# Kernel tuning notes

Measured on AMD Instinct MI355X. Metric: run time of the kernel, lower is better.

## Reference

```python
import jax, jax.numpy as jnp
import numpy as np
import math

B, L, S, E, D = 32, 2048, 2048, 64, 64

def setup_inputs() -> dict:
    key = jax.random.key(0)
    kq, kk, kv = jax.random.split(key, 3)
    return {
        "queries": jax.random.normal(kq, (B, L, E), dtype=jnp.float32),
        "keys":    jax.random.normal(kk, (B, S, E), dtype=jnp.float32),
        "values":  jax.random.normal(kv, (B, S, D), dtype=jnp.float32),
    }

def reference(queries, keys, values):
    # scale = 1/sqrt(E) since self.scale is None
    scale = 1.0 / math.sqrt(queries.shape[-1])
    # unfused QK^T -> softmax -> V (dropout is identity at inference)
    scores = jnp.einsum('ble,bse->bls', queries, keys)  # [B,L,S]
    # mask_flag branch not taken because L == S (matches torch code path)
    A = jax.nn.softmax(scale * scores, axis=-1)
    V = jnp.einsum('bls,bsd->bld', A, values)  # [B,L,D]
    return V
```

## Files before the change

### kernel.cpp

```cpp
#include <hip/hip_runtime.h>
#include <hip/hip_bf16.h>


#define B_ 32
#define L_ 2048
#define S_ 2048
#define E_ 64
#define D_ 64
#define BQ 128
#define NIMG 32
#define IMG_BYTES 16384
#define NCHUNK 16

typedef __attribute__((ext_vector_type(8))) short bf16x8;
typedef __attribute__((ext_vector_type(16))) float f32x16;
typedef __attribute__((ext_vector_type(4))) unsigned u32x4;

__device__ __forceinline__ unsigned short f2b(float f) {
  unsigned u = __builtin_bit_cast(unsigned, f);
  u += 0x7fff + ((u >> 16) & 1);
  return (unsigned short)(u >> 16);
}

__device__ __forceinline__ unsigned pk2(float a, float b) {
#if defined(__has_builtin) && __has_builtin(__builtin_amdgcn_cvt_pk_bf16_f32)
  typedef __bf16 b2 __attribute__((ext_vector_type(2)));
  b2 t = __builtin_amdgcn_cvt_pk_bf16_f32(a, b);
  return __builtin_bit_cast(unsigned, t);
#else
  return (unsigned)f2b(a) | ((unsigned)f2b(b) << 16);
#endif
}

__device__ __forceinline__ float fexp2(float x) {
#if defined(__has_builtin) && __has_builtin(__builtin_amdgcn_exp2f)
  return __builtin_amdgcn_exp2f(x);
#else
  return exp2f(x);
#endif
}

__device__ __forceinline__ void cp16(const void* g, void* lbase) {
#if defined(__has_builtin) && __has_builtin(__builtin_amdgcn_global_load_lds)
  typedef const __attribute__((address_space(1))) void gvoid;
  typedef __attribute__((address_space(3))) void lvoid;
  __builtin_amdgcn_global_load_lds((gvoid*)g, (lvoid*)lbase, 16, 0, 0);
#endif
}

__global__ __launch_bounds__(256) void prepass(
    const float* __restrict__ K, const float* __restrict__ V,
    char* __restrict__ ws) {
  const int tid  = threadIdx.x;
  const int lane = tid & 63;
  const int quad = lane >> 4;
  const int qb0  = quad & 1;
  const int qb1  = (quad >> 1) & 1;

  const int b  = blockIdx.x >> 5;
  const int c  = blockIdx.x & 31;
  const int s0 = c * 64;

  const float* Kb = K + (long)b * S_ * E_;
  const float* Vb = V + (long)b * S_ * D_;
  short* img = (short*)(ws + (size_t)blockIdx.x * IMG_BYTES);

#pragma unroll
  for (int it = 0; it < 4; ++it) {
    const int i  = tid + it * 256;
    const int s  = i >> 4;
    const int c4 = (i & 15) << 2;

    float4 kv = *(const float4*)(Kb + (long)(s0 + s) * E_ + c4);
    {
      int g = ((c4 >> 3) + s) & 7;
      *(uint2*)&img[s * 64 + g * 8 + (c4 & 7)] = make_uint2(pk2(kv.x, kv.y), pk2(kv.z, kv.w));
    }

    float4 vv = *(const float4*)(Vb + (long)(s0 + s) * D_ + c4);
    float a0 = vv.x, a1 = vv.y, a2 = vv.z, a3 = vv.w;
    float s0f = qb1 ? a0 : a2;
    float s1f = qb1 ? a1 : a3;
    float r0  = __shfl_xor(s0f, 32);
    float r1  = __shfl_xor(s1f, 32);
    float b0 = qb1 ? r0 : a0;
    float b1 = qb1 ? r1 : a1;
    float b2 = qb1 ? a2 : r0;
    float b3 = qb1 ? a3 : r1;
    float t0 = qb0 ? b0 : b1;
    float t1 = qb0 ? b2 : b3;
    float u0 = __shfl_xor(t0, 16);
    float u1 = __shfl_xor(t1, 16);
    float w0 = qb0 ? u0 : b0;
    float w1 = qb0 ? b1 : u0;
    float w2 = qb0 ? u1 : b2;
    float w3 = qb0 ? b3 : u1;
    const int base = s - quad;
    const int d    = c4 + quad;
    int g = ((base >> 3) + d) & 7;
    *(uint2*)&img[4096 + d * 64 + g * 8 + (base & 7)] = make_uint2(pk2(w0, w1), pk2(w2, w3));
  }
}

__global__ __launch_bounds__(512, 4) void attn_fwd(
    const float* __restrict__ Q, const char* __restrict__ ws,
    float* __restrict__ O) {
  __shared__ __align__(16) char smem[65536 + 1024];
  float* Obuf = (float*)smem;
  float* ML   = (float*)(smem + 65536);

  const int tid  = threadIdx.x;
  const int lane = tid & 63;
  const int wv   = tid >> 6;
  const int l31  = lane & 31;
  const int h    = lane >> 5;
  const int qg   = wv >> 1;
  const int kh   = wv & 1;

  const int b  = blockIdx.x >> 4;
  const int q0 = (blockIdx.x & 15) * BQ;

  const float SCALE2 = 0.125f * 1.44269504088896340736f;
  const char* img0 = ws + (size_t)b * ((size_t)NIMG * IMG_BYTES);

#pragma unroll
  for (int j = 0; j < 4; ++j)
    cp16(img0 + wv * 4096 + j * 1024 + lane * 16, smem + wv * 4096 + j * 1024);

  bf16x8 qf[4];
  {
    const float* qrow = Q + ((long)b * L_ + q0 + qg * 32 + l31) * E_;
#pragma unroll
    for (int ke = 0; ke < 4; ++ke) {
      const float* sp = qrow + ke * 16 + h * 8;
      float4 x = *(const float4*)(sp);
      float4 y = *(const float4*)(sp + 4);
      u32x4 uu = { pk2(x.x * SCALE2, x.y * SCALE2), pk2(x.z * SCALE2, x.w * SCALE2),
                   pk2(y.x * SCALE2, y.y * SCALE2), pk2(y.z * SCALE2, y.w * SCALE2) };
      qf[ke] = __builtin_bit_cast(bf16x8, uu);
    }
  }

  int pl = l31;
  {
    const int blk = (pl >> 2) & 3;
    if (blk == 1) pl += 4;
    else if (blk == 2) pl -= 4;
  }

  int offK[2][4];
#pragma unroll
  for (int nt = 0; nt < 2; ++nt) {
    const int row = nt * 32 + pl;
#pragma unroll
    for (int ke = 0; ke < 4; ++ke)
      offK[nt][ke] = kh * 16384 + row * 128 + (((ke * 2 + h) + row) & 7) * 16;
  }
  int offV[2][4];
#pragma unroll
  for (int mt = 0; mt < 2; ++mt) {
    const int d = mt * 32 + l31;
#pragma unroll
    for (int ks = 0; ks < 4; ++ks)
      offV[mt][ks] = kh * 16384 + 8192 + d * 128 + (((ks * 2 + h) + d) & 7) * 16;
  }

  f32x16 o[2];
#pragma unroll
  for (int mt = 0; mt < 2; ++mt)
#pragma unroll
    for (int r = 0; r < 16; ++r) o[mt][r] = 0.f;
  float lrun = 0.f;

  __syncthreads();

#define CHUNK_BODY(TT, BUFB, OTHB)                                             \
  {                                                                            \
    if ((TT) + 1 < NCHUNK) {                                                   \
      const char* img = img0 + (size_t)((TT) + 1) * 32768;                     \
      _Pragma("unroll")                                                        \
      for (int j = 0; j < 4; ++j)                                              \
        cp16(img + wv * 4096 + j * 1024 + lane * 16,                           \
             smem + (OTHB) + wv * 4096 + j * 1024);                            \
    }                                                                          \
    _Pragma("unroll")                                                          \
    for (int nt = 0; nt < 2; ++nt) {                                           \
      bf16x8 kf[4];                                                            \
      _Pragma("unroll")                                                        \
      for (int ke = 0; ke < 4; ++ke)                                           \
        kf[ke] = *(const bf16x8*)(smem + (BUFB) + offK[nt][ke]);               \
      f32x16 acc;                                                              \
      _Pragma("unroll")                                                        \
      for (int r = 0; r < 16; ++r) acc[r] = 0.f;                               \
      _Pragma("unroll")                                                        \
      for (int ke = 0; ke < 4; ++ke)                                           \
        acc = __builtin_amdgcn_mfma_f32_32x32x16_bf16(kf[ke], qf[ke], acc,     \
                                                      0, 0, 0);                \
      float pr[16];                                                            \
      _Pragma("unroll")                                                        \
      for (int r = 0; r < 16; ++r) pr[r] = fexp2(acc[r]);                      \
      float rsa = 0.f, rsb = 0.f;                                              \
      _Pragma("unroll")                                                        \
      for (int r = 0; r < 8; ++r) { rsa += pr[2 * r]; rsb += pr[2 * r + 1]; }  \
      lrun += rsa + rsb;                                                       \
      u32x4 f0 = { pk2(pr[0], pr[1]), pk2(pr[2], pr[3]),                       \
                   pk2(pr[4], pr[5]), pk2(pr[6], pr[7]) };                     \
      bf16x8 pf0 = __builtin_bit_cast(bf16x8, f0);                             \
      u32x4 f1 = { pk2(pr[8], pr[9]), pk2(pr[10], pr[11]),                     \
                   pk2(pr[12], pr[13]), pk2(pr[14], pr[15]) };                 \
      bf16x8 pf1 = __builtin_bit_cast(bf16x8, f1);                             \
      _Pragma("unroll")                                                        \
      for (int mt = 0; mt < 2; ++mt) {                                         \
        bf16x8 vf0 = *(const bf16x8*)(smem + (BUFB) + offV[mt][nt * 2 + 0]);   \
        o[mt] = __builtin_amdgcn_mfma_f32_32x32x16_bf16(vf0, pf0, o[mt],       \
                                                        0, 0, 0);              \
        bf16x8 vf1 = *(const bf16x8*)(smem + (BUFB) + offV[mt][nt * 2 + 1]);   \
        o[mt] = __builtin_amdgcn_mfma_f32_32x32x16_bf16(vf1, pf1, o[mt],       \
                                                        0, 0, 0);              \
      }                                                                        \
    }                                                                          \
    __syncthreads();                                                           \
  }

  for (int t = 0; t < NCHUNK; t += 2) {
    CHUNK_BODY(t, 0, 32768)
    CHUNK_BODY(t + 1, 32768, 0)
  }
#undef CHUNK_BODY

  float lt = lrun + __shfl_xor(lrun, 32);

  if (lane < 32)
    ML[(qg * 2 + kh) * 32 + l31] = lt;
  __syncthreads();

  const float inv = 1.f / (lt + ML[(qg * 2 + (kh ^ 1)) * 32 + l31]);
  const int q = qg * 32 + l31;

  if (kh == 1) {
#pragma unroll
    for (int mt = 0; mt < 2; ++mt)
#pragma unroll
      for (int r = 0; r < 16; ++r) {
        const int d = mt * 32 + (r & 3) + 8 * (r >> 2) + 4 * h;
        Obuf[q * 68 + d] = o[mt][r];
      }
  }
  __syncthreads();

  if (kh == 0) {
#pragma unroll
    for (int mt = 0; mt < 2; ++mt)
#pragma unroll
      for (int r = 0; r < 16; ++r) {
        const int d = mt * 32 + (r & 3) + 8 * (r >> 2) + 4 * h;
        Obuf[q * 68 + d] = (o[mt][r] + Obuf[q * 68 + d]) * inv;
      }
  }
  __syncthreads();

  {
    const int qq = tid >> 2;
    const int dh = (tid & 3) * 16;
    float* orow = O + ((long)b * L_ + q0 + qq) * D_ + dh;
    const float* src = &Obuf[qq * 68 + dh];
#pragma unroll
    for (int j = 0; j < 4; ++j)
      *(float4*)(orow + j * 4) = *(const float4*)(src + j * 4);
  }
}

extern "C" void kernel_launch(void* const* d_in, const int* in_sizes, int n_in,
                              void* d_out, int out_size, void* d_ws, size_t ws_size,
                              hipStream_t stream) {
  const float* Q = (const float*)d_in[0];
  const float* K = (const float*)d_in[1];
  const float* V = (const float*)d_in[2];
  float* O = (float*)d_out;

  prepass<<<dim3(B_ * NIMG), dim3(256), 0, stream>>>(K, V, (char*)d_ws);
  attn_fwd<<<dim3(B_ * (L_ / BQ)), dim3(512), 0, stream>>>(Q, (const char*)d_ws, O);
}
```

Baseline: 150.2 us.

## Replace barrier double-buffering with flag-synced 4-stage producer/consumer LDS ring

Each tile now holds 64 keys, split across the two key-halves, instead of two images per stage. A 4-buffer LDS ring is managed by per-buffer ready and consumed counters in shared memory instead of block-wide __syncthreads. A rotating producer wave waits for a buffer to be drained, then issues global_load_lds for the chunk four steps ahead and sets its ready flag. The K/V swizzle changes from additive to XOR so LDS addresses reduce to XORs of a base offset. The aim is to drop per-chunk full-block barriers and let waves drift apart. The spin-waits rely on volatile LDS polling and the order of s_waitcnt, which risks stalls or races.

```diff
diff --git a/kernel.cpp b/kernel.cpp
--- a/kernel.cpp
+++ b/kernel.cpp
@@ -10,7 +10,8 @@
 #define BQ 128
 #define NIMG 32
 #define IMG_BYTES 16384
-#define NCHUNK 16
+#define NCHUNK 32
+#define NBUF 4
 
 typedef __attribute__((ext_vector_type(8))) short bf16x8;
 typedef __attribute__((ext_vector_type(16))) float f32x16;
@@ -48,6 +49,10 @@
 #endif
 }
 
+__device__ __forceinline__ void wait_ge(const volatile int* p, int want) {
+  while (*p < want) __builtin_amdgcn_s_sleep(1);
+}
+
 __global__ __launch_bounds__(256) void prepass(
     const float* __restrict__ K, const float* __restrict__ V,
     char* __restrict__ ws) {
@@ -73,7 +78,7 @@
 
     float4 kv = *(const float4*)(Kb + (long)(s0 + s) * E_ + c4);
     {
-      int g = ((c4 >> 3) + s) & 7;
+      int g = (c4 >> 3) ^ (s & 7);
       *(uint2*)&img[s * 64 + g * 8 + (c4 & 7)] = make_uint2(pk2(kv.x, kv.y), pk2(kv.z, kv.w));
     }
 
@@ -97,7 +102,7 @@
     float w3 = qb0 ? b3 : u1;
     const int base = s - quad;
     const int d    = c4 + quad;
-    int g = ((base >> 3) + d) & 7;
+    int g = (base >> 3) ^ (d & 7);
     *(uint2*)&img[4096 + d * 64 + g * 8 + (base & 7)] = make_uint2(pk2(w0, w1), pk2(w2, w3));
   }
 }
@@ -105,9 +110,10 @@
 __global__ __launch_bounds__(512, 4) void attn_fwd(
     const float* __restrict__ Q, const char* __restrict__ ws,
     float* __restrict__ O) {
-  __shared__ __align__(16) char smem[65536 + 1024];
+  __shared__ __align__(16) char smem[65536 + 1024 + 64];
   float* Obuf = (float*)smem;
   float* ML   = (float*)(smem + 65536);
+  int*   sync = (int*)(smem + 66560);
 
   const int tid  = threadIdx.x;
   const int lane = tid & 63;
@@ -123,9 +129,15 @@
   const float SCALE2 = 0.125f * 1.44269504088896340736f;
   const char* img0 = ws + (size_t)b * ((size_t)NIMG * IMG_BYTES);
 
-#pragma unroll
-  for (int j = 0; j < 4; ++j)
-    cp16(img0 + wv * 4096 + j * 1024 + lane * 16, smem + wv * 4096 + j * 1024);
+  if (tid < 8) sync[tid] = 0;
+  __syncthreads();
+
+  if (wv < 4) {
+    const char* img = img0 + (size_t)wv * IMG_BYTES;
+#pragma unroll
+    for (int j = 0; j < 16; ++j)
+      cp16(img + j * 1024 + lane * 16, smem + wv * 16384 + j * 1024);
+  }
 
   bf16x8 qf[4];
   {
@@ -141,6 +153,11 @@
     }
   }
 
+  if (wv < 4) {
+    asm volatile("s_waitcnt vmcnt(0)" ::: "memory");
+    if (lane == 0) ((volatile int*)sync)[wv] = 1;
+  }
+
   int pl = l31;
   {
     const int blk = (pl >> 2) & 3;
@@ -148,22 +165,8 @@
     else if (blk == 2) pl -= 4;
   }
 
-  int offK[2][4];
-#pragma unroll
-  for (int nt = 0; nt < 2; ++nt) {
-    const int row = nt * 32 + pl;
-#pragma unroll
-    for (int ke = 0; ke < 4; ++ke)
-      offK[nt][ke] = kh * 16384 + row * 128 + (((ke * 2 + h) + row) & 7) * 16;
-  }
-  int offV[2][4];
-#pragma unroll
-  for (int mt = 0; mt < 2; ++mt) {
-    const int d = mt * 32 + l31;
-#pragma unroll
-    for (int ks = 0; ks < 4; ++ks)
-      offV[mt][ks] = kh * 16384 + 8192 + d * 128 + (((ks * 2 + h) + d) & 7) * 16;
-  }
+  const int kb = (kh << 12) + (pl << 7) + ((h ^ (pl & 7)) << 4);
+  const int vb = 8192 + (l31 << 7) + (((kh * 4 + h) ^ (l31 & 7)) << 4);
 
   f32x16 o[2];
 #pragma unroll
@@ -172,61 +175,65 @@
     for (int r = 0; r < 16; ++r) o[mt][r] = 0.f;
   float lrun = 0.f;
 
-  __syncthreads();
-
-#define CHUNK_BODY(TT, BUFB, OTHB)                                             \
-  {                                                                            \
-    if ((TT) + 1 < NCHUNK) {                                                   \
-      const char* img = img0 + (size_t)((TT) + 1) * 32768;                     \
-      _Pragma("unroll")                                                        \
-      for (int j = 0; j < 4; ++j)                                              \
-        cp16(img + wv * 4096 + j * 1024 + lane * 16,                           \
-             smem + (OTHB) + wv * 4096 + j * 1024);                            \
-    }                                                                          \
-    _Pragma("unroll")                                                          \
-    for (int nt = 0; nt < 2; ++nt) {                                           \
-      bf16x8 kf[4];                                                            \
-      _Pragma("unroll")                                                        \
-      for (int ke = 0; ke < 4; ++ke)                                           \
-        kf[ke] = *(const bf16x8*)(smem + (BUFB) + offK[nt][ke]);               \
-      f32x16 acc;                                                              \
-      _Pragma("unroll")                                                        \
-      for (int r = 0; r < 16; ++r) acc[r] = 0.f;                               \
-      _Pragma("unroll")                                                        \
-      for (int ke = 0; ke < 4; ++ke)                                           \
-        acc = __builtin_amdgcn_mfma_f32_32x32x16_bf16(kf[ke], qf[ke], acc,     \
-                                                      0, 0, 0);                \
-      float pr[16];                                                            \
-      _Pragma("unroll")                                                        \
-      for (int r = 0; r < 16; ++r) pr[r] = fexp2(acc[r]);                      \
-      float rsa = 0.f, rsb = 0.f;                                              \
-      _Pragma("unroll")                                                        \
-      for (int r = 0; r < 8; ++r) { rsa += pr[2 * r]; rsb += pr[2 * r + 1]; }  \
-      lrun += rsa + rsb;                                                       \
-      u32x4 f0 = { pk2(pr[0], pr[1]), pk2(pr[2], pr[3]),                       \
-                   pk2(pr[4], pr[5]), pk2(pr[6], pr[7]) };                     \
-      bf16x8 pf0 = __builtin_bit_cast(bf16x8, f0);                             \
-      u32x4 f1 = { pk2(pr[8], pr[9]), pk2(pr[10], pr[11]),                     \
-                   pk2(pr[12], pr[13]), pk2(pr[14], pr[15]) };                 \
-      bf16x8 pf1 = __builtin_bit_cast(bf16x8, f1);                             \
-      _Pragma("unroll")                                                        \
-      for (int mt = 0; mt < 2; ++mt) {                                         \
-        bf16x8 vf0 = *(const bf16x8*)(smem + (BUFB) + offV[mt][nt * 2 + 0]);   \
-        o[mt] = __builtin_amdgcn_mfma_f32_32x32x16_bf16(vf0, pf0, o[mt],       \
-                                                        0, 0, 0);              \
-        bf16x8 vf1 = *(const bf16x8*)(smem + (BUFB) + offV[mt][nt * 2 + 1]);   \
-        o[mt] = __builtin_amdgcn_mfma_f32_32x32x16_bf16(vf1, pf1, o[mt],       \
-                                                        0, 0, 0);              \
-      }                                                                        \
-    }                                                                          \
-    __syncthreads();                                                           \
-  }
-
-  for (int t = 0; t < NCHUNK; t += 2) {
-    CHUNK_BODY(t, 0, 32768)
-    CHUNK_BODY(t + 1, 32768, 0)
-  }
-#undef CHUNK_BODY
+  for (int t = 0; t < NCHUNK; ++t) {
+    const int s = t & 3;
+    wait_ge((volatile int*)&sync[s], (t >> 2) + 1);
+    asm volatile("" ::: "memory");
+
+    const int bufb = s << 14;
+    const int kbuf = kb ^ bufb;
+    const int vbuf = vb ^ bufb;
+
+    bf16x8 kf[4];
+#pragma unroll
+    for (int ke = 0; ke < 4; ++ke)
+      kf[ke] = *(const bf16x8*)(smem + (kbuf ^ (ke << 5)));
+    f32x16 acc;
+#pragma unroll
+    for (int r = 0; r < 16; ++r) acc[r] = 0.f;
+#pragma unroll
+    for (int ke = 0; ke < 4; ++ke)
+      acc = __builtin_amdgcn_mfma_f32_32x32x16_bf16(kf[ke], qf[ke], acc, 0, 0, 0);
+
+    u32x4 f0, f1;
+#pragma unroll
+    for (int g = 0; g < 4; ++g) {
+      float p0 = fexp2(acc[2 * g]);
+      float p1 = fexp2(acc[2 * g + 1]);
+      lrun += p0 + p1;
+      f0[g] = pk2(p0, p1);
+      float p2 = fexp2(acc[8 + 2 * g]);
+      float p3 = fexp2(acc[8 + 2 * g + 1]);
+      lrun += p2 + p3;
+      f1[g] = pk2(p2, p3);
+    }
+    bf16x8 pf0 = __builtin_bit_cast(bf16x8, f0);
+    bf16x8 pf1 = __builtin_bit_cast(bf16x8, f1);
+
+#pragma unroll
+    for (int mt = 0; mt < 2; ++mt) {
+      bf16x8 vf0 = *(const bf16x8*)(smem + (vbuf ^ (mt << 12)));
+      o[mt] = __builtin_amdgcn_mfma_f32_32x32x16_bf16(vf0, pf0, o[mt], 0, 0, 0);
+      bf16x8 vf1 = *(const bf16x8*)(smem + (vbuf ^ (mt << 12) ^ (1 << 5)));
+      o[mt] = __builtin_amdgcn_mfma_f32_32x32x16_bf16(vf1, pf1, o[mt], 0, 0, 0);
+    }
+
+    asm volatile("s_waitcnt lgkmcnt(0)" ::: "memory");
+    if (lane == 0) atomicAdd(&sync[4 + s], 1);
+
+    const int tp = t + 4;
+    if (tp < NCHUNK && (tp & 7) == wv) {
+      const int sp_ = tp & 3;
+      wait_ge((volatile int*)&sync[4 + sp_], (tp >> 2) * 8);
+      asm volatile("" ::: "memory");
+      const char* img = img0 + (size_t)tp * IMG_BYTES;
+#pragma unroll
+      for (int j = 0; j < 16; ++j)
+        cp16(img + j * 1024 + lane * 16, smem + sp_ * 16384 + j * 1024);
+      asm volatile("s_waitcnt vmcnt(0)" ::: "memory");
+      if (lane == 0) ((volatile int*)sync)[sp_] = (tp >> 2) + 1;
+    }
+  }
 
   float lt = lrun + __shfl_xor(lrun, 32);
 
```

Result: no change. 150.2 us (-0.0%).
